# Kernel optimization log

Measured on AMD Instinct MI355X. Metric: run time of the kernel, lower is better.

The kernel has to match this reference:

```python
import jax, jax.numpy as jnp
import numpy as np

D_MODEL = 1024
H = 16
D_K = D_MODEL // H
MASK_VALUE = -2000000000.0  # fp32 path in the original module


def setup_inputs() -> dict:
    key = jax.random.key(0)
    ks = jax.random.split(key, 7)
    B, S = 2, 2048
    scale = 1.0 / np.sqrt(D_MODEL)
    inp = {
        "q": jax.random.normal(ks[0], (B, S, D_MODEL), jnp.float32),
        "k": jax.random.normal(ks[1], (B, S, D_MODEL), jnp.float32),
        "v": jax.random.normal(ks[2], (B, S, D_MODEL), jnp.float32),
        # causal mask, broadcast over batch and heads
        "mask": jnp.tril(jnp.ones((1, 1, S, S), jnp.int32)),
        "w_q": jax.random.normal(ks[3], (D_MODEL, D_MODEL), jnp.float32) * scale,
        "w_k": jax.random.normal(ks[4], (D_MODEL, D_MODEL), jnp.float32) * scale,
        "w_v": jax.random.normal(ks[5], (D_MODEL, D_MODEL), jnp.float32) * scale,
        "w_o": jax.random.normal(ks[6], (D_MODEL, D_MODEL), jnp.float32) * scale,
    }
    return inp


def reference(q, k, v, mask, w_q, w_k, w_v, w_o):
    B, S, _ = q.shape
    # Linear(d_model, d_model, bias=False): x @ W.T  (weights stored [out, in])
    def proj(x, w):
        y = jnp.einsum('bsd,ed->bse', x, w)
        return y.reshape(B, -1, H, D_K).transpose(0, 2, 1, 3)  # [B, H, S, d_k]

    Q = proj(q, w_q)
    K = proj(k, w_k)
    V = proj(v, w_v)

    scores = jnp.einsum('bhsd,bhtd->bhst', Q, K) * (D_K ** -0.5)  # [B,H,S,S]
    scores = jnp.where(mask == 0, MASK_VALUE, scores)
    attn = jax.nn.softmax(scores, axis=-1)
    x = jnp.einsum('bhst,bhtd->bhsd', attn, V)                     # [B,H,S,d_k]
    x = x.transpose(0, 2, 1, 3).reshape(B, -1, D_MODEL)            # [B,S,d_model]
    return jnp.einsum('bsd,ed->bse', x, w_o)
```

## Files before the change

kernel.cpp:

```cpp
#include <hip/hip_runtime.h>
#include <math.h>

#define S_LEN 2048
#define DM 1024
#define NH 16
#define DK 64
#define BATCH 2
#define MS (BATCH*S_LEN)

typedef __attribute__((ext_vector_type(8))) short bf16x8;
typedef __attribute__((ext_vector_type(4))) float f32x4;
typedef __attribute__((ext_vector_type(16))) float f32x16;
typedef unsigned short u16;
typedef unsigned int u32;

__device__ __forceinline__ u16 f2b(float f) {
  union { float f; u32 u; } x; x.f = f;
  u32 r = x.u + 0x7FFFu + ((x.u >> 16) & 1u);
  return (u16)(r >> 16);
}

__device__ __forceinline__ u32 cvtpk_bf16(float lo, float hi) {
  u32 r;
  asm volatile("v_cvt_pk_bf16_f32 %0, %1, %2" : "=v"(r) : "v"(lo), "v"(hi));
  return r;
}

struct CvtArgs {
  const float* src[7];
  u16* dst[7];
  float scl[7];
  int n4[7];
};

__global__ void cvt_all(CvtArgs a) {
  const int seg = blockIdx.y;
  const float* __restrict__ in = a.src[seg];
  u16* __restrict__ out = a.dst[seg];
  const float s = a.scl[seg];
  const int n4 = a.n4[seg];
  int idx = blockIdx.x * blockDim.x + threadIdx.x;
  int stride = gridDim.x * blockDim.x;
  for (int i = idx; i < n4; i += stride) {
    float4 v = ((const float4*)in)[i];
    ushort4 o;
    o.x = f2b(v.x * s); o.y = f2b(v.y * s); o.z = f2b(v.z * s); o.w = f2b(v.w * s);
    ((ushort4*)out)[i] = o;
  }
}

__device__ __forceinline__ void gload_lds16(const u16* g, u16* l) {
  __builtin_amdgcn_global_load_lds((const __attribute__((address_space(1))) u32*)g,
                                   (__attribute__((address_space(3))) u32*)l, 16, 0, 0);
}

template<bool OUT_BF16, int BM>
__device__ __forceinline__ void gemm_body(
    const u16* __restrict__ A, const u16* __restrict__ B, void* __restrict__ Cout,
    int M, int N, int K, int bx, int by, u16* lsA, u16* lsB)
{
  constexpr int MF = BM / 32;
  const int tid = threadIdx.x;
  const int lane = tid & 63;
  const int wid = tid >> 6;
  const int wr = wid >> 1, wc = wid & 1;
  const int m0 = by * BM, n0 = bx * 128;

  f32x4 acc[MF][4];
#pragma unroll
  for (int i = 0; i < MF; ++i)
#pragma unroll
    for (int j = 0; j < 4; ++j) acc[i][j] = (f32x4){0.f, 0.f, 0.f, 0.f};

  const int ntiles = K >> 6;

#define GSTAGE(K0) do { \
    _Pragma("unroll") \
    for (int i = 0; i < BM/32; ++i) { \
      int u = tid + i * 256; \
      int row = u >> 3, c8 = u & 7; \
      gload_lds16(A + (size_t)(m0 + row) * K + (K0) + ((c8 ^ (row & 7)) * 8), &lsA[u * 8]); \
    } \
    _Pragma("unroll") \
    for (int i = 0; i < 4; ++i) { \
      int u = tid + i * 256; \
      int row = u >> 3, c8 = u & 7; \
      gload_lds16(B + (size_t)(n0 + row) * K + (K0) + ((c8 ^ (row & 7)) * 8), &lsB[u * 8]); \
    } \
  } while (0)

  GSTAGE(0);
  const int ksel = lane >> 4;
  for (int kt = 0; kt < ntiles; ++kt) {
    __syncthreads();
    bf16x8 af[2][MF], bfr[2][4];
#pragma unroll
    for (int kk = 0; kk < 2; ++kk) {
#pragma unroll
      for (int m = 0; m < MF; ++m) {
        int row = wr * (BM/2) + m * 16 + (lane & 15);
        af[kk][m] = *(const bf16x8*)&lsA[row * 64 + (((kk * 4 + ksel) ^ (row & 7)) * 8)];
      }
#pragma unroll
      for (int n = 0; n < 4; ++n) {
        int row = wc * 64 + n * 16 + (lane & 15);
        bfr[kk][n] = *(const bf16x8*)&lsB[row * 64 + (((kk * 4 + ksel) ^ (row & 7)) * 8)];
      }
    }
    __syncthreads();
    if (kt + 1 < ntiles) GSTAGE((kt + 1) << 6);
#pragma unroll
    for (int kk = 0; kk < 2; ++kk)
#pragma unroll
      for (int m = 0; m < MF; ++m)
#pragma unroll
        for (int n = 0; n < 4; ++n)
          acc[m][n] = __builtin_amdgcn_mfma_f32_16x16x32_bf16(af[kk][m], bfr[kk][n], acc[m][n], 0, 0, 0);
  }
#undef GSTAGE

  const int rbase = m0 + wr * (BM/2) + ((lane >> 4) << 2);
  const int cbase = n0 + wc * 64 + (lane & 15);
#pragma unroll
  for (int m = 0; m < MF; ++m)
#pragma unroll
    for (int n = 0; n < 4; ++n)
#pragma unroll
      for (int j = 0; j < 4; ++j) {
        int r = rbase + m * 16 + j;
        int c = cbase + n * 16;
        if (OUT_BF16)
          ((u16*)Cout)[(size_t)r * N + c] = f2b(acc[m][n][j]);
        else
          ((float*)Cout)[(size_t)r * N + c] = acc[m][n][j];
      }
}

struct G3Args {
  const u16* A[3];
  const u16* B[3];
  u16* C[3];
};

__global__ __launch_bounds__(256) void gemm_qkv(G3Args g) {
  __shared__ u16 lsA[128*64];
  __shared__ u16 lsB[128*64];
  const int bid = blockIdx.x;
  const int gi = bid >> 8;
  const int f = bid & 255;
  const int gx = (gi == 2) ? 32 : 8;
  const int N = (gi == 2) ? MS : DM;
  const int M = (gi == 2) ? DM : MS;
  gemm_body<true,128>(g.A[gi], g.B[gi], g.C[gi], M, N, DM,
                      f % gx, f / gx, lsA, lsB);
}

__global__ __launch_bounds__(256) void gemm_out(
    const u16* __restrict__ A, const u16* __restrict__ B, float* __restrict__ C) {
  __shared__ u16 lsA[64*64];
  __shared__ u16 lsB[128*64];
  gemm_body<false,64>(A, B, C, MS, DM, DM, blockIdx.x, blockIdx.y, lsA, lsB);
}

__global__ __launch_bounds__(256) void attn_fwd(
    const u16* __restrict__ Qp, const u16* __restrict__ Kp, const u16* __restrict__ Vt,
    u16* __restrict__ AO)
{
  __shared__ __align__(16) u16 lds_kv[4][4096];
  __shared__ float lds_l[4][2][32];
  const int tid = threadIdx.x;
  const int lane = tid & 63;
  const int w = tid >> 6;
  const int ql = lane & 31;
  const int h = lane >> 5;
  const int bid = blockIdx.x;
  const int j = 63 - (bid >> 5);
  const int bh = bid & 31;
  const int b = bh >> 4;
  const int hh = bh & 15;
  const int q0 = j * 32;
  const int qg = q0 + ql;
  const size_t baseQK = (size_t)b * S_LEN * DM + hh * DK;
  const size_t baseV  = (size_t)hh * DK * MS + (size_t)b * S_LEN;

  u16* const lk = lds_kv[w];
  u16* const lv = lds_kv[w] + 2048;

  bf16x8 qf[4];
#pragma unroll
  for (int ks = 0; ks < 4; ++ks)
    qf[ks] = *(const bf16x8*)&Qp[baseQK + (size_t)qg * DM + ks * 16 + h * 8];
  asm volatile("s_waitcnt vmcnt(0)" ::: "memory");

  f32x16 ot[2];
#pragma unroll
  for (int n = 0; n < 2; ++n)
#pragma unroll
    for (int r = 0; r < 16; ++r) ot[n][r] = 0.f;
  float lrun = 0.f;

#define STAGE_K(KV0) do { \
    _Pragma("unroll") \
    for (int jj = 0; jj < 4; ++jj) { \
      int c = jj * 64 + lane; \
      int kr = c >> 3, kc = c & 7; \
      gload_lds16(Kp + baseQK + (size_t)((KV0) + kr) * DM + ((kc ^ (kr & 7)) * 8), &lk[c * 8]); \
    } \
  } while (0)

#define STAGE_V(KV0) do { \
    _Pragma("unroll") \
    for (int jj = 0; jj < 4; ++jj) { \
      int c = jj * 64 + lane; \
      int vr = c >> 2, vc = c & 3; \
      gload_lds16(Vt + baseV + (size_t)vr * MS + (KV0) + ((vc ^ (vr & 3)) * 8), &lv[c * 8]); \
    } \
  } while (0)

  if (w <= j) { STAGE_K(w * 32); STAGE_V(w * 32); }

  for (int tt = w; tt <= j; tt += 4) {
    const bool nx = (tt + 4 <= j);
    asm volatile("s_waitcnt vmcnt(4)" ::: "memory");
    bf16x8 kf[4];
#pragma unroll
    for (int ks = 0; ks < 4; ++ks)
      kf[ks] = *(const bf16x8*)&lk[(ql * 8 + ((2 * ks + h) ^ (ql & 7))) * 8];
    asm volatile("s_waitcnt lgkmcnt(0)" ::: "memory");
    if (nx) STAGE_K((tt + 4) * 32);

    f32x16 st;
#pragma unroll
    for (int r = 0; r < 16; ++r) st[r] = 0.f;
    __builtin_amdgcn_s_setprio(1);
#pragma unroll
    for (int ks = 0; ks < 4; ++ks)
      st = __builtin_amdgcn_mfma_f32_32x32x16_bf16(kf[ks], qf[ks], st, 0, 0, 0);
    __builtin_amdgcn_s_setprio(0);

    if (tt == j) {
#pragma unroll
      for (int r = 0; r < 16; ++r) {
        int kvg = tt * 32 + (r & 3) + 8 * (r >> 2) + 4 * h;
        if (kvg > qg) st[r] = -1e30f;
      }
    }

#pragma unroll
    for (int r = 0; r < 16; ++r) {
      float p_ = st[r];
      asm("v_exp_f32 %0, %1" : "=v"(p_) : "v"(p_));
      st[r] = p_;
    }
    {
      float t0 = st[0] + st[1], t1 = st[2] + st[3];
      float t2 = st[4] + st[5], t3 = st[6] + st[7];
      float t4 = st[8] + st[9], t5 = st[10] + st[11];
      float t6 = st[12] + st[13], t7 = st[14] + st[15];
      float u0 = t0 + t1, u1 = t2 + t3, u2 = t4 + t5, u3 = t6 + t7;
      lrun += (u0 + u1) + (u2 + u3);
    }

    if (nx) { asm volatile("s_waitcnt vmcnt(4)" ::: "memory"); }
    else    { asm volatile("s_waitcnt vmcnt(0)" ::: "memory"); }
    bf16x8 vf[2][2];
#pragma unroll
    for (int n = 0; n < 2; ++n)
#pragma unroll
      for (int kst = 0; kst < 2; ++kst)
        vf[n][kst] = *(const bf16x8*)&lv[((n * 32 + ql) * 4 + ((2 * kst + h) ^ (ql & 3))) * 8];
    asm volatile("s_waitcnt lgkmcnt(0)" ::: "memory");
    if (nx) STAGE_V((tt + 4) * 32);

#pragma unroll
    for (int kst = 0; kst < 2; ++kst) {
      u32 pkg[4];
#pragma unroll
      for (int g4 = 0; g4 < 4; ++g4)
        pkg[g4] = cvtpk_bf16(st[8 * kst + 2 * g4], st[8 * kst + 2 * g4 + 1]);
      asm("v_permlane32_swap_b32 %0, %1" : "+v"(pkg[0]), "+v"(pkg[2]));
      asm("v_permlane32_swap_b32 %0, %1" : "+v"(pkg[1]), "+v"(pkg[3]));
      union { u32 u[4]; bf16x8 v; } pb;
      pb.u[0] = pkg[0]; pb.u[1] = pkg[1]; pb.u[2] = pkg[2]; pb.u[3] = pkg[3];
      __builtin_amdgcn_s_setprio(1);
#pragma unroll
      for (int n = 0; n < 2; ++n)
        ot[n] = __builtin_amdgcn_mfma_f32_32x32x16_bf16(vf[n][kst], pb.v, ot[n], 0, 0, 0);
      __builtin_amdgcn_s_setprio(0);
    }
  }

  lds_l[w][h][ql] = lrun;

  {
    float* comb = (float*)lds_kv[w];
#pragma unroll
    for (int n = 0; n < 2; ++n)
#pragma unroll
      for (int r = 0; r < 16; ++r) {
        int d = 32 * n + (r & 3) + 8 * (r >> 2) + 4 * h;
        comb[d * 32 + (ql ^ (d & 31))] = ot[n][r];
      }
  }
  __syncthreads();
  {
    const int q = tid >> 3;
    const int d0 = (tid & 7) * 8;
    float lsum = 0.f;
#pragma unroll
    for (int w2 = 0; w2 < 4; ++w2)
      lsum += lds_l[w2][0][q] + lds_l[w2][1][q];
    float inv = 1.0f / lsum;
    const float* c0 = (const float*)lds_kv[0];
    const float* c1 = (const float*)lds_kv[1];
    const float* c2 = (const float*)lds_kv[2];
    const float* c3 = (const float*)lds_kv[3];
    u32 o4[4];
#pragma unroll
    for (int ii = 0; ii < 4; ++ii) {
      int da = d0 + 2 * ii, db = da + 1;
      int ia = da * 32 + (q ^ (da & 31));
      int ib = db * 32 + (q ^ (db & 31));
      float va = c0[ia] + c1[ia] + c2[ia] + c3[ia];
      float vb = c0[ib] + c1[ib] + c2[ib] + c3[ib];
      o4[ii] = cvtpk_bf16(va * inv, vb * inv);
    }
    uint4 outv;
    outv.x = o4[0]; outv.y = o4[1]; outv.z = o4[2]; outv.w = o4[3];
    *(uint4*)&AO[baseQK + (size_t)(q0 + q) * DM + d0] = outv;
  }
#undef STAGE_K
#undef STAGE_V
}

extern "C" void kernel_launch(void* const* d_in, const int* in_sizes, int n_in,
                              void* d_out, int out_size, void* d_ws, size_t ws_size,
                              hipStream_t stream) {
  const float* q  = (const float*)d_in[0];
  const float* k  = (const float*)d_in[1];
  const float* v  = (const float*)d_in[2];
  const float* wq = (const float*)d_in[4];
  const float* wk = (const float*)d_in[5];
  const float* wv = (const float*)d_in[6];
  const float* wo = (const float*)d_in[7];

  const size_t nIn = (size_t)MS * DM;
  const size_t nW  = (size_t)DM * DM;

  u16* ws = (u16*)d_ws;
  u16* qb  = ws; ws += nIn;
  u16* kb  = ws; ws += nIn;
  u16* vb  = ws; ws += nIn;
  u16* wqb = ws; ws += nW;
  u16* wkb = ws; ws += nW;
  u16* wvb = ws; ws += nW;
  u16* wob = ws; ws += nW;
  u16* Qp  = ws; ws += nIn;
  u16* Kp  = ws; ws += nIn;
  u16* Vt  = ws; ws += nIn;
  u16* AO  = ws; ws += nIn;

  CvtArgs ca;
  const float QSCL = 0.125f * 1.44269504089f;
  ca.src[0] = q;  ca.dst[0] = qb;  ca.n4[0] = (int)(nIn / 4); ca.scl[0] = 1.f;
  ca.src[1] = k;  ca.dst[1] = kb;  ca.n4[1] = (int)(nIn / 4); ca.scl[1] = 1.f;
  ca.src[2] = v;  ca.dst[2] = vb;  ca.n4[2] = (int)(nIn / 4); ca.scl[2] = 1.f;
  ca.src[3] = wq; ca.dst[3] = wqb; ca.n4[3] = (int)(nW / 4);  ca.scl[3] = QSCL;
  ca.src[4] = wk; ca.dst[4] = wkb; ca.n4[4] = (int)(nW / 4);  ca.scl[4] = 1.f;
  ca.src[5] = wv; ca.dst[5] = wvb; ca.n4[5] = (int)(nW / 4);  ca.scl[5] = 1.f;
  ca.src[6] = wo; ca.dst[6] = wob; ca.n4[6] = (int)(nW / 4);  ca.scl[6] = 1.f;
  cvt_all<<<dim3(256, 7), 256, 0, stream>>>(ca);

  G3Args g3;
  g3.A[0] = qb;  g3.B[0] = wqb; g3.C[0] = Qp;
  g3.A[1] = kb;  g3.B[1] = wkb; g3.C[1] = Kp;
  g3.A[2] = wvb; g3.B[2] = vb;  g3.C[2] = Vt;
  gemm_qkv<<<dim3(768), 256, 0, stream>>>(g3);

  attn_fwd<<<dim3(64 * 32), 256, 0, stream>>>(Qp, Kp, Vt, AO);

  gemm_out<<<dim3(8, 64), 256, 0, stream>>>(AO, wob, (float*)d_out);
}
```

Before: 112.7 us.

## Double-buffer GEMM K-tiles with vmcnt-based waits and halve tile depth

The shared GEMM body now uses a two-stage LDS ring with 32-wide K tiles instead of a single 64-wide buffer. Prefetch runs two tiles ahead, and explicit s_waitcnt vmcnt plus raw s_barrier replace __syncthreads, so global-to-LDS loads overlap MFMA work. The XOR swizzle on LDS rows is dropped, which may bring back bank conflicts on the 64-byte row stride, and there are twice as many barriers per K.

```diff
diff --git a/kernel.cpp b/kernel.cpp
--- a/kernel.cpp
+++ b/kernel.cpp
@@ -24,6 +24,10 @@
   u32 r;
   asm volatile("v_cvt_pk_bf16_f32 %0, %1, %2" : "=v"(r) : "v"(lo), "v"(hi));
   return r;
+}
+
+template<int N> __device__ __forceinline__ void waitcnt_vm() {
+  asm volatile("s_waitcnt vmcnt(%0)" :: "n"(N) : "memory");
 }
 
 struct CvtArgs {
@@ -60,6 +64,7 @@
     int M, int N, int K, int bx, int by, u16* lsA, u16* lsB)
 {
   constexpr int MF = BM / 32;
+  constexpr int SL = BM / 64 + 2;
   const int tid = threadIdx.x;
   const int lane = tid & 63;
   const int wid = tid >> 6;
@@ -72,50 +77,49 @@
 #pragma unroll
     for (int j = 0; j < 4; ++j) acc[i][j] = (f32x4){0.f, 0.f, 0.f, 0.f};
 
-  const int ntiles = K >> 6;
-
-#define GSTAGE(K0) do { \
+  const int ntiles = K >> 5;
+
+#define GSTAGE(BUF, K0) do { \
+    u16* dA_ = lsA + (BUF) * (BM * 32); \
+    u16* dB_ = lsB + (BUF) * (128 * 32); \
     _Pragma("unroll") \
-    for (int i = 0; i < BM/32; ++i) { \
+    for (int i = 0; i < BM/64; ++i) { \
       int u = tid + i * 256; \
-      int row = u >> 3, c8 = u & 7; \
-      gload_lds16(A + (size_t)(m0 + row) * K + (K0) + ((c8 ^ (row & 7)) * 8), &lsA[u * 8]); \
+      gload_lds16(A + (size_t)(m0 + (u >> 2)) * K + (K0) + (u & 3) * 8, &dA_[u * 8]); \
     } \
     _Pragma("unroll") \
-    for (int i = 0; i < 4; ++i) { \
+    for (int i = 0; i < 2; ++i) { \
       int u = tid + i * 256; \
-      int row = u >> 3, c8 = u & 7; \
-      gload_lds16(B + (size_t)(n0 + row) * K + (K0) + ((c8 ^ (row & 7)) * 8), &lsB[u * 8]); \
+      gload_lds16(B + (size_t)(n0 + (u >> 2)) * K + (K0) + (u & 3) * 8, &dB_[u * 8]); \
     } \
   } while (0)
 
-  GSTAGE(0);
-  const int ksel = lane >> 4;
+  GSTAGE(0, 0);
+  if (1 < ntiles) GSTAGE(1, 32);
+  int cur = 0;
   for (int kt = 0; kt < ntiles; ++kt) {
-    __syncthreads();
-    bf16x8 af[2][MF], bfr[2][4];
-#pragma unroll
-    for (int kk = 0; kk < 2; ++kk) {
-#pragma unroll
-      for (int m = 0; m < MF; ++m) {
-        int row = wr * (BM/2) + m * 16 + (lane & 15);
-        af[kk][m] = *(const bf16x8*)&lsA[row * 64 + (((kk * 4 + ksel) ^ (row & 7)) * 8)];
-      }
-#pragma unroll
-      for (int n = 0; n < 4; ++n) {
-        int row = wc * 64 + n * 16 + (lane & 15);
-        bfr[kk][n] = *(const bf16x8*)&lsB[row * 64 + (((kk * 4 + ksel) ^ (row & 7)) * 8)];
-      }
-    }
-    __syncthreads();
-    if (kt + 1 < ntiles) GSTAGE((kt + 1) << 6);
-#pragma unroll
-    for (int kk = 0; kk < 2; ++kk)
-#pragma unroll
-      for (int m = 0; m < MF; ++m)
-#pragma unroll
-        for (int n = 0; n < 4; ++n)
-          acc[m][n] = __builtin_amdgcn_mfma_f32_16x16x32_bf16(af[kk][m], bfr[kk][n], acc[m][n], 0, 0, 0);
+    if (kt + 1 < ntiles) waitcnt_vm<SL>();
+    else                 waitcnt_vm<0>();
+    __builtin_amdgcn_s_barrier();
+    bf16x8 af[MF], bfr[4];
+    const int kOff = (lane >> 4) * 8;
+    const u16* sA = lsA + cur * (BM * 32);
+    const u16* sB = lsB + cur * (128 * 32);
+#pragma unroll
+    for (int m = 0; m < MF; ++m)
+      af[m] = *(const bf16x8*)&sA[(wr * (BM/2) + m * 16 + (lane & 15)) * 32 + kOff];
+#pragma unroll
+    for (int n = 0; n < 4; ++n)
+      bfr[n] = *(const bf16x8*)&sB[(wc * 64 + n * 16 + (lane & 15)) * 32 + kOff];
+    asm volatile("s_waitcnt lgkmcnt(0)" ::: "memory");
+    __builtin_amdgcn_s_barrier();
+    if (kt + 2 < ntiles) GSTAGE(cur, (kt + 2) << 5);
+#pragma unroll
+    for (int m = 0; m < MF; ++m)
+#pragma unroll
+      for (int n = 0; n < 4; ++n)
+        acc[m][n] = __builtin_amdgcn_mfma_f32_16x16x32_bf16(af[m], bfr[n], acc[m][n], 0, 0, 0);
+    cur ^= 1;
   }
 #undef GSTAGE
 
@@ -143,8 +147,8 @@
 };
 
 __global__ __launch_bounds__(256) void gemm_qkv(G3Args g) {
-  __shared__ u16 lsA[128*64];
-  __shared__ u16 lsB[128*64];
+  __shared__ u16 lsA[2 * 128 * 32];
+  __shared__ u16 lsB[2 * 128 * 32];
   const int bid = blockIdx.x;
   const int gi = bid >> 8;
   const int f = bid & 255;
@@ -157,8 +161,8 @@
 
 __global__ __launch_bounds__(256) void gemm_out(
     const u16* __restrict__ A, const u16* __restrict__ B, float* __restrict__ C) {
-  __shared__ u16 lsA[64*64];
-  __shared__ u16 lsB[128*64];
+  __shared__ u16 lsA[2 * 64 * 32];
+  __shared__ u16 lsB[2 * 128 * 32];
   gemm_body<false,64>(A, B, C, MS, DM, DM, blockIdx.x, blockIdx.y, lsA, lsB);
 }
 
```

New measurement: 125.4 us. +11.3%, slower.
